# Kernel tuning notes

Measured on AMD Instinct MI355X. Metric: run time of the kernel, lower is better.

The kernel has to match this reference:

```python
import jax, jax.numpy as jnp
import numpy as np

DIM_MODEL = 512
DIM_HEAD = 64


def setup_inputs() -> dict:
    key = jax.random.key(0)
    ks = jax.random.split(key, 7)
    B, S = 4, 4096
    x = jax.random.normal(ks[0], (B, S, DIM_MODEL), dtype=jnp.float32)
    mask = jnp.ones((B, 1, S), dtype=jnp.int32)
    # torch Linear init: U(-1/sqrt(fan_in), 1/sqrt(fan_in)); stored as (in, out) for x @ W
    bound = 1.0 / np.sqrt(DIM_MODEL)
    Wq = jax.random.uniform(ks[1], (DIM_MODEL, DIM_HEAD), minval=-bound, maxval=bound, dtype=jnp.float32)
    bq = jax.random.uniform(ks[2], (DIM_HEAD,), minval=-bound, maxval=bound, dtype=jnp.float32)
    Wk = jax.random.uniform(ks[3], (DIM_MODEL, DIM_HEAD), minval=-bound, maxval=bound, dtype=jnp.float32)
    bk = jax.random.uniform(ks[4], (DIM_HEAD,), minval=-bound, maxval=bound, dtype=jnp.float32)
    Wv = jax.random.uniform(ks[5], (DIM_MODEL, DIM_HEAD), minval=-bound, maxval=bound, dtype=jnp.float32)
    bv = jax.random.uniform(ks[6], (DIM_HEAD,), minval=-bound, maxval=bound, dtype=jnp.float32)
    return {"x": x, "mask": mask, "Wq": Wq, "bq": bq, "Wk": Wk, "bk": bk, "Wv": Wv, "bv": bv}


def reference(x, mask, Wq, bq, Wk, bk, Wv, bv):
    # single-head QKV projection
    q = x @ Wq + bq  # (B, S, Dh)
    k = x @ Wk + bk
    v = x @ Wv + bv
    dot_scale = jnp.sqrt(jnp.float32(DIM_HEAD))
    # explicit O(S^2) score matrix, softmax over keys
    scores = jnp.einsum("bqd,bkd->bqk", q, k) / dot_scale  # (B, S, S)
    attn = jax.nn.softmax(scores, axis=-1)
    # faithful to source: mask applied AFTER softmax with -inf fill
    attn = jnp.where(mask == 0, jnp.float32(-jnp.inf), attn)
    return jnp.einsum("bqk,bkd->bqd", attn, v)  # (B, S, Dh)
```

## Files before the change

kernel.cpp:

```cpp
#include <hip/hip_runtime.h>
#include <hip/hip_bf16.h>

typedef _Float16 half8v __attribute__((ext_vector_type(8)));
typedef _Float16 half4v __attribute__((ext_vector_type(4)));
typedef _Float16 half2v __attribute__((ext_vector_type(2)));
typedef __fp16   fp16x2 __attribute__((ext_vector_type(2)));
typedef __attribute__((ext_vector_type(4))) float floatx4;

#define LOG2E_OVER_8 0.18033688011112042f


__global__ __launch_bounds__(256) void wtrans_k(const float* __restrict__ Wq,
                                                const float* __restrict__ Wk,
                                                const float* __restrict__ Wv,
                                                _Float16* __restrict__ Wt) {
    int idx = blockIdx.x * 256 + threadIdx.x;
    int p = idx >> 15, rem = idx & 32767;
    int k = rem >> 6;
    int n = rem & 63;
    const float* W = (p == 0) ? Wq : ((p == 1) ? Wk : Wv);
    int ctg = p * 4 + (n >> 4), m = n & 15;
    int kc = k >> 5, quad = (k >> 3) & 3, j = k & 7;
    Wt[(((ctg << 4) + kc) * 64 + (quad << 4) + m) * 8 + j] = (_Float16)W[k * 64 + n];
}

#define XS_STRIDE 536
__global__ __launch_bounds__(256) void proj_k(const float* __restrict__ x,
                                              const _Float16* __restrict__ Wt,
                                              const float* __restrict__ bq,
                                              const float* __restrict__ bk,
                                              const float* __restrict__ bv,
                                              _Float16* __restrict__ Qh,
                                              _Float16* __restrict__ Kh,
                                              _Float16* __restrict__ Vh) {
    __shared__ _Float16 xs[2][16 * XS_STRIDE];

    int tid = threadIdx.x, l = tid & 63, wv = tid >> 6;
    int m = l & 15, quad = l >> 4;
    int row0 = blockIdx.x * 32;

#pragma unroll
    for (int s = 0; s < 2; s++)
#pragma unroll
        for (int i = 0; i < 8; i++) {
            int idx = tid + i * 256;
            int row = idx >> 7, c4 = idx & 127;
            float4 v = *(const float4*)(x + (row0 + s * 16 + row) * 512 + c4 * 4);
            union { half2v h[2]; uint2 u; } cv;
            cv.h[0][0] = (_Float16)v.x; cv.h[0][1] = (_Float16)v.y;
            cv.h[1][0] = (_Float16)v.z; cv.h[1][1] = (_Float16)v.w;
            *(uint2*)(xs[s] + row * XS_STRIDE + c4 * 4) = cv.u;
        }
    __syncthreads();

    const _Float16* arow0 = xs[0] + m * XS_STRIDE + quad * 8;
    const _Float16* arow1 = xs[1] + m * XS_STRIDE + quad * 8;

    floatx4 acc[2][3];
#pragma unroll
    for (int s = 0; s < 2; s++)
#pragma unroll
        for (int i = 0; i < 3; i++) acc[s][i] = (floatx4)(0.f);

#pragma unroll 4
    for (int kc = 0; kc < 16; kc++) {
        half8v a0 = *(const half8v*)(arow0 + kc * 32);
        half8v a1 = *(const half8v*)(arow1 + kc * 32);
#pragma unroll
        for (int ct = 0; ct < 3; ct++) {
            int ctg = wv * 3 + ct;
            half8v b = *(const half8v*)(Wt + (((ctg << 4) + kc) * 64 + l) * 8);
            acc[0][ct] = __builtin_amdgcn_mfma_f32_16x16x32_f16(a0, b, acc[0][ct], 0, 0, 0);
            acc[1][ct] = __builtin_amdgcn_mfma_f32_16x16x32_f16(a1, b, acc[1][ct], 0, 0, 0);
        }
    }

#pragma unroll
    for (int s = 0; s < 2; s++) {
        int rowb = row0 + s * 16;
#pragma unroll
        for (int ct = 0; ct < 3; ct++) {
            int ctg = wv * 3 + ct;
            int col = ctg * 16 + m;
            float bias = (ctg < 4) ? bq[col] : ((ctg < 8) ? bk[col - 64] : bv[col - 128]);
            if (ctg < 8) {
                _Float16* dst = (ctg < 4) ? Qh : Kh;
                float scl = (ctg < 4) ? LOG2E_OVER_8 : 1.0f;
                int dd = (ctg & 3) * 16 + m;
                int c = dd >> 5, quadQ = (dd >> 3) & 3, j = dd & 7;
#pragma unroll
                for (int r = 0; r < 4; r++) {
                    int row = rowb + quad * 4 + r;
                    int chunk = ((row >> 4) << 1) + c;
                    dst[(chunk * 64 + quadQ * 16 + (row & 15)) * 8 + j] =
                        (_Float16)((acc[s][ct][r] + bias) * scl);
                }
            } else {
                int dt = ctg - 8;
                int t64 = rowb >> 6, ktp = (rowb >> 5) & 1, half = (rowb >> 4) & 1;
                int chunk = t64 * 8 + dt * 2 + ktp;
                union { _Float16 h[4]; unsigned long long u; } pk;
#pragma unroll
                for (int r = 0; r < 4; r++) pk.h[r] = (_Float16)(acc[s][ct][r] + bias);
                *(unsigned long long*)(Vh + (chunk * 64 + quad * 16 + m) * 8 + half * 4) = pk.u;
            }
        }
    }
}

template <int NT>
__global__ __launch_bounds__(256) void attn_k(const _Float16* __restrict__ Qh,
                                              const _Float16* __restrict__ Kh,
                                              const _Float16* __restrict__ Vh,
                                              const int* __restrict__ mask,
                                              _Float16* __restrict__ Np,
                                              float* __restrict__ Dp,
                                              int gshift) {
    __shared__ float T[4][16 * 68];

    int tid = threadIdx.x, l = tid & 63, wv = tid >> 6;
    int m = l & 15, quad = l >> 4;
    int bid = blockIdx.x;
    int grp = bid & ((1 << gshift) - 1), qblk = bid >> gshift;
    int os = grp >> 2, b = grp & 3;
    int q0 = qblk * 128 + wv * 32;

    const int* maskb = mask + b * 4096 + os * (NT * 64);
    int az = 0;
#pragma unroll
    for (int i = 0; i < NT; i++) az |= (maskb[l + i * 64] == 0);
    const bool hasz = __any(az);

    int qt_g = (b * 4096 + q0) >> 4;
    half8v qf[2][2];
#pragma unroll
    for (int qt = 0; qt < 2; qt++)
#pragma unroll
        for (int c = 0; c < 2; c++)
            qf[qt][c] = *(const half8v*)(Qh + (((qt_g + qt) * 2 + c) * 64 + l) * 8);

    int tb0 = (b * 64 + os * NT) * 512;
    const uint4* kh4 = (const uint4*)Kh + tb0;
    const uint4* vh4 = (const uint4*)Vh + tb0;

    floatx4 oacc[2][4];
#pragma unroll
    for (int qt = 0; qt < 2; qt++)
#pragma unroll
        for (int dt = 0; dt < 4; dt++) oacc[qt][dt] = (floatx4)(0.f);
    float dl[2] = {0.f, 0.f};

#pragma unroll 2
    for (int t = 0; t < NT; t++) {
        const uint4* kt4 = kh4 + t * 512;
        const uint4* vt4 = vh4 + t * 512;
        uint4 vv[4];
#pragma unroll
        for (int sub = 0; sub < 4; sub++) {
            union { uint4 u; half8v h; } ku0, ku1;
            ku0.u = kt4[(sub * 2 + 0) * 64 + l];
            ku1.u = kt4[(sub * 2 + 1) * 64 + l];
            if ((sub & 1) == 0) {
#pragma unroll
                for (int dt = 0; dt < 4; dt++)
                    vv[dt] = vt4[(dt * 2 + (sub >> 1)) * 64 + l];
            }
            half4v pb[2];
#pragma unroll
            for (int qt = 0; qt < 2; qt++) {
                floatx4 sf = (floatx4)(0.f);
                sf = __builtin_amdgcn_mfma_f32_16x16x32_f16(ku0.h, qf[qt][0], sf, 0, 0, 0);
                sf = __builtin_amdgcn_mfma_f32_16x16x32_f16(ku1.h, qf[qt][1], sf, 0, 0, 0);
                float p0 = exp2f(sf[0]), p1 = exp2f(sf[1]);
                float p2 = exp2f(sf[2]), p3 = exp2f(sf[3]);
                dl[qt] += (p0 + p1) + (p2 + p3);
                if (hasz) {
                    int kg = t * 64 + sub * 16 + quad * 4;
                    if (maskb[kg + 0] == 0) p0 = -__builtin_inff();
                    if (maskb[kg + 1] == 0) p1 = -__builtin_inff();
                    if (maskb[kg + 2] == 0) p2 = -__builtin_inff();
                    if (maskb[kg + 3] == 0) p3 = -__builtin_inff();
                }
                union { fp16x2 h[2]; half4v h4; } pu;
                pu.h[0] = __builtin_amdgcn_cvt_pkrtz(p0, p1);
                pu.h[1] = __builtin_amdgcn_cvt_pkrtz(p2, p3);
                pb[qt] = pu.h4;
            }
#pragma unroll
            for (int dt = 0; dt < 4; dt++) {
                union { uint4 u; half4v h[2]; } vc; vc.u = vv[dt];
                half4v va = vc.h[sub & 1];
                oacc[0][dt] = __builtin_amdgcn_mfma_f32_16x16x16f16(va, pb[0], oacc[0][dt], 0, 0, 0);
                oacc[1][dt] = __builtin_amdgcn_mfma_f32_16x16x16f16(va, pb[1], oacc[1][dt], 0, 0, 0);
            }
        }
    }

    float* Tw = &T[wv][0];
    int rowb = os * 16384 + b * 4096 + q0;
#pragma unroll
    for (int qt = 0; qt < 2; qt++) {
        float dqt = dl[qt];
        dqt += __shfl_xor(dqt, 16, 64);
        dqt += __shfl_xor(dqt, 32, 64);
        if (l < 16) Dp[rowb + qt * 16 + l] = dqt;
#pragma unroll
        for (int dt = 0; dt < 4; dt++)
#pragma unroll
            for (int r = 0; r < 4; r++)
                Tw[m * 68 + dt * 16 + quad * 4 + r] = oacc[qt][dt][r];
        __builtin_amdgcn_s_waitcnt(0);
#pragma unroll
        for (int g = 0; g < 4; g++) {
            int idx = g * 64 + l;
            int row = idx >> 4, c4 = (idx & 15) * 4;
            float4 v = *(const float4*)(Tw + row * 68 + c4);
            union { half4v h; unsigned long long u; } pk;
            pk.h[0] = (_Float16)v.x; pk.h[1] = (_Float16)v.y;
            pk.h[2] = (_Float16)v.z; pk.h[3] = (_Float16)v.w;
            *(unsigned long long*)(Np + (size_t)(rowb + qt * 16 + row) * 64 + c4) = pk.u;
        }
        __builtin_amdgcn_s_waitcnt(0);
    }
}

__global__ __launch_bounds__(256) void combine_k(const _Float16* __restrict__ Np,
                                                 const float* __restrict__ Dp,
                                                 float* __restrict__ out,
                                                 int spl) {
    int g4 = blockIdx.x * 256 + threadIdx.x;
    int row = g4 >> 4;
    float4 nu = make_float4(0.f, 0.f, 0.f, 0.f);
    float d = 0.f;
    for (int sp = 0; sp < spl; sp++) {
        union { unsigned long long u; half4v h; } v;
        v.u = *(const unsigned long long*)(Np + ((size_t)sp << 20) + (size_t)g4 * 4);
        nu.x += (float)v.h[0]; nu.y += (float)v.h[1];
        nu.z += (float)v.h[2]; nu.w += (float)v.h[3];
        d += Dp[sp * 16384 + row];
    }
    float inv = 1.0f / d;
    ((float4*)out)[g4] = make_float4(nu.x * inv, nu.y * inv, nu.z * inv, nu.w * inv);
}

extern "C" void kernel_launch(void* const* d_in, const int* in_sizes, int n_in,
                              void* d_out, int out_size, void* d_ws, size_t ws_size,
                              hipStream_t stream) {
    const float* x  = (const float*)d_in[0];
    const int* mask = (const int*)d_in[1];
    const float* Wq = (const float*)d_in[2];
    const float* bq = (const float*)d_in[3];
    const float* Wk = (const float*)d_in[4];
    const float* bk = (const float*)d_in[5];
    const float* Wv = (const float*)d_in[6];
    const float* bv = (const float*)d_in[7];
    float* out = (float*)d_out;

    char* ws = (char*)d_ws;
    _Float16* Wt = (_Float16*)(ws);
    _Float16* Qh = (_Float16*)(ws + 0x40000);
    _Float16* Kh = (_Float16*)(ws + 0x240000);
    _Float16* Vh = (_Float16*)(ws + 0x440000);
    float*    Dp = (float*)(ws + 0x640000);
    _Float16* Np = (_Float16*)(ws + 0x740000);

    size_t need16 = 0x740000 + (size_t)16 * 16384 * 64 * 2;
    int spl = (ws_size >= need16) ? 16 : 8;

    wtrans_k<<<384, 256, 0, stream>>>(Wq, Wk, Wv, Wt);
    proj_k<<<512, 256, 0, stream>>>(x, Wt, bq, bk, bv, Qh, Kh, Vh);
    if (spl == 16)
        attn_k<4><<<32 * 64, 256, 0, stream>>>(Qh, Kh, Vh, mask, Np, Dp, 6);
    else
        attn_k<8><<<32 * 32, 256, 0, stream>>>(Qh, Kh, Vh, mask, Np, Dp, 5);
    combine_k<<<1024, 256, 0, stream>>>(Np, Dp, out, spl);
}
```

Measured before the change: 137.5 us.

## Load x directly into MFMA fragments and reduce attention key-split count

The projection kernel stops staging x through shared memory. Each lane now reads its fp32 A-fragment straight from global memory and converts it to fp16 in registers, which removes the LDS writes and the block barrier. The attention launch is fixed to a 4-way key split with a larger template parameter (fewer, bigger blocks) instead of a 16- or 8-way split chosen by workspace size. That shrinks partial-result traffic and combine work, but gives less parallelism across the GPU.

```diff
diff --git a/kernel.cpp b/kernel.cpp
--- a/kernel.cpp
+++ b/kernel.cpp
@@ -24,7 +24,6 @@
     Wt[(((ctg << 4) + kc) * 64 + (quad << 4) + m) * 8 + j] = (_Float16)W[k * 64 + n];
 }
 
-#define XS_STRIDE 536
 __global__ __launch_bounds__(256) void proj_k(const float* __restrict__ x,
                                               const _Float16* __restrict__ Wt,
                                               const float* __restrict__ bq,
@@ -33,28 +32,12 @@
                                               _Float16* __restrict__ Qh,
                                               _Float16* __restrict__ Kh,
                                               _Float16* __restrict__ Vh) {
-    __shared__ _Float16 xs[2][16 * XS_STRIDE];
-
     int tid = threadIdx.x, l = tid & 63, wv = tid >> 6;
     int m = l & 15, quad = l >> 4;
     int row0 = blockIdx.x * 32;
 
-#pragma unroll
-    for (int s = 0; s < 2; s++)
-#pragma unroll
-        for (int i = 0; i < 8; i++) {
-            int idx = tid + i * 256;
-            int row = idx >> 7, c4 = idx & 127;
-            float4 v = *(const float4*)(x + (row0 + s * 16 + row) * 512 + c4 * 4);
-            union { half2v h[2]; uint2 u; } cv;
-            cv.h[0][0] = (_Float16)v.x; cv.h[0][1] = (_Float16)v.y;
-            cv.h[1][0] = (_Float16)v.z; cv.h[1][1] = (_Float16)v.w;
-            *(uint2*)(xs[s] + row * XS_STRIDE + c4 * 4) = cv.u;
-        }
-    __syncthreads();
-
-    const _Float16* arow0 = xs[0] + m * XS_STRIDE + quad * 8;
-    const _Float16* arow1 = xs[1] + m * XS_STRIDE + quad * 8;
+    const float* xr0 = x + (row0 + m) * 512 + quad * 8;
+    const float* xr1 = x + (row0 + 16 + m) * 512 + quad * 8;
 
     floatx4 acc[2][3];
 #pragma unroll
@@ -64,14 +47,25 @@
 
 #pragma unroll 4
     for (int kc = 0; kc < 16; kc++) {
-        half8v a0 = *(const half8v*)(arow0 + kc * 32);
-        half8v a1 = *(const half8v*)(arow1 + kc * 32);
+        float4 a0a = *(const float4*)(xr0 + kc * 32);
+        float4 a0b = *(const float4*)(xr0 + kc * 32 + 4);
+        float4 a1a = *(const float4*)(xr1 + kc * 32);
+        float4 a1b = *(const float4*)(xr1 + kc * 32 + 4);
+        union { _Float16 h[8]; half8v v; } A0, A1;
+        A0.h[0] = (_Float16)a0a.x; A0.h[1] = (_Float16)a0a.y;
+        A0.h[2] = (_Float16)a0a.z; A0.h[3] = (_Float16)a0a.w;
+        A0.h[4] = (_Float16)a0b.x; A0.h[5] = (_Float16)a0b.y;
+        A0.h[6] = (_Float16)a0b.z; A0.h[7] = (_Float16)a0b.w;
+        A1.h[0] = (_Float16)a1a.x; A1.h[1] = (_Float16)a1a.y;
+        A1.h[2] = (_Float16)a1a.z; A1.h[3] = (_Float16)a1a.w;
+        A1.h[4] = (_Float16)a1b.x; A1.h[5] = (_Float16)a1b.y;
+        A1.h[6] = (_Float16)a1b.z; A1.h[7] = (_Float16)a1b.w;
 #pragma unroll
         for (int ct = 0; ct < 3; ct++) {
             int ctg = wv * 3 + ct;
             half8v b = *(const half8v*)(Wt + (((ctg << 4) + kc) * 64 + l) * 8);
-            acc[0][ct] = __builtin_amdgcn_mfma_f32_16x16x32_f16(a0, b, acc[0][ct], 0, 0, 0);
-            acc[1][ct] = __builtin_amdgcn_mfma_f32_16x16x32_f16(a1, b, acc[1][ct], 0, 0, 0);
+            acc[0][ct] = __builtin_amdgcn_mfma_f32_16x16x32_f16(A0.v, b, acc[0][ct], 0, 0, 0);
+            acc[1][ct] = __builtin_amdgcn_mfma_f32_16x16x32_f16(A1.v, b, acc[1][ct], 0, 0, 0);
         }
     }
 
@@ -264,14 +258,8 @@
     float*    Dp = (float*)(ws + 0x640000);
     _Float16* Np = (_Float16*)(ws + 0x740000);
 
-    size_t need16 = 0x740000 + (size_t)16 * 16384 * 64 * 2;
-    int spl = (ws_size >= need16) ? 16 : 8;
-
     wtrans_k<<<384, 256, 0, stream>>>(Wq, Wk, Wv, Wt);
     proj_k<<<512, 256, 0, stream>>>(x, Wt, bq, bk, bv, Qh, Kh, Vh);
-    if (spl == 16)
-        attn_k<4><<<32 * 64, 256, 0, stream>>>(Qh, Kh, Vh, mask, Np, Dp, 6);
-    else
-        attn_k<8><<<32 * 32, 256, 0, stream>>>(Qh, Kh, Vh, mask, Np, Dp, 5);
-    combine_k<<<1024, 256, 0, stream>>>(Np, Dp, out, spl);
-}
+    attn_k<16><<<32 * 16, 256, 0, stream>>>(Qh, Kh, Vh, mask, Np, Dp, 4);
+    combine_k<<<1024, 256, 0, stream>>>(Np, Dp, out, 4);
+}
```

New measurement: 147.7 us. 7.4% more time.
